# Kernel optimization log

Hardware: AMD Instinct MI355X
Metric: run time of the kernel (lower is better)

Reference implementation:

```python
import jax, jax.numpy as jnp
import numpy as np

N = 50000      # node_size
D = 256        # node_F == rel_F (ent_F)
R = 1000       # rel_size
E = 300000     # triple_size == n_edges
DEPTH = 2
KSEL = E // 2  # rows rewritten by W_orth transform
NPROXY = 128


def l2n(x):
    # tf.nn.l2_normalize with eps=1e-12
    return x * jax.lax.rsqrt(jnp.maximum(jnp.sum(x * x, axis=-1, keepdims=True), 1e-12))


def setup_inputs() -> dict:
    key = jax.random.key(0)
    ks = jax.random.split(key, 12)
    features = jax.random.normal(ks[0], (N, D), jnp.float32)
    rel_emb = jax.random.normal(ks[1], (R, D), jnp.float32)
    p = jax.random.normal(ks[2], (N, 1), jnp.float32)            # dynamic_node_kernel
    w_keys = jax.random.normal(ks[3], (DEPTH, D, D), jnp.float32) / np.float32(np.sqrt(D))
    attn_kernels = jax.random.normal(ks[4], (DEPTH, D, 1), jnp.float32) * 0.1
    proxy = jax.random.normal(ks[5], (NPROXY, D * (DEPTH + 1)), jnp.float32) * 0.05
    gate_kernel = jax.random.normal(ks[6], (D * (DEPTH + 1), D * (DEPTH + 1)), jnp.float32) / np.float32(np.sqrt(D * (DEPTH + 1)))
    adj_row = jnp.sort(jax.random.randint(ks[7], (E,), 0, N))    # destination (segment) ids, sorted
    adj_col = jax.random.randint(ks[8], (E,), 0, N)              # neighbor ids
    rel_ids = jax.random.randint(ks[9], (E,), 0, R)              # relation id per triple/edge
    rel_vals = jax.random.uniform(ks[10], (E,), jnp.float32)     # sparse_val per triple
    new_indices = jax.random.randint(ks[11], (KSEL,), 0, E)      # rows updated by w_key
    return dict(features=features, rel_emb=rel_emb, p=p, w_keys=w_keys,
                attn_kernels=attn_kernels, proxy=proxy, gate_kernel=gate_kernel,
                rel_vals=rel_vals, adj_row=adj_row, adj_col=adj_col,
                rel_ids=rel_ids, new_indices=new_indices)


def reference(features, rel_emb, p, w_keys, attn_kernels, proxy, gate_kernel,
              rel_vals, adj_row, adj_col, rel_ids, new_indices):
    tanh_p = jnp.tanh(p)                                   # [N,1]
    feats = features * tanh_p                              # use_p scaling (activation=None -> identity)
    outputs = [feats]
    for l in range(DEPTH):
        # sparse (triple,rel) x rel_emb : one relation per triple -> gather + scale
        rels_sum = rel_vals[:, None] * rel_emb[rel_ids]    # [E,D]
        rels_sum = l2n(rels_sum)
        # W_orth: transform a subset of rows by w_key, scatter back
        src = rels_sum[new_indices] @ w_keys[l]            # [KSEL,D]
        rels_sum = rels_sum.at[new_indices].set(src)
        neighs = feats[adj_col]                            # [E,D] gather
        rels_sum = rels_sum * tanh_p[adj_col]              # use_p on neighbors
        # Householder-style reflection of neighbor features
        neighs = neighs - 2.0 * jnp.sum(neighs * rels_sum, axis=1, keepdims=True) * rels_sum
        # per-edge attention logits, softmax over incoming edges of each row node
        att = (rels_sum @ attn_kernels[l])[:, 0]           # [E]
        m = jax.ops.segment_max(att, adj_row, num_segments=N)      # [N]
        att = jnp.exp(att - m[adj_row])
        s = jax.ops.segment_sum(att, adj_row, num_segments=N)      # [N]
        att = att / s[adj_row]
        # weighted scatter-aggregate
        feats = jax.ops.segment_sum(neighs * att[:, None], adj_row, num_segments=N)  # [N,D]
        feats = feats * tanh_p
        outputs.append(feats)
    out = jnp.concatenate(outputs, axis=-1)                # [N, D*(DEPTH+1)]
    proxy_att = jax.nn.softmax(l2n(out) @ l2n(proxy).T, axis=-1)   # [N,128]
    proxy_feature = out - proxy_att @ proxy
    gate = jax.nn.sigmoid(proxy_feature @ gate_kernel)
    out = gate * out + (1.0 - gate) * proxy_feature
    return (out, p)
```

## Files before the change

### kernel.cpp

```cpp
#include <hip/hip_runtime.h>
#include <math.h>

#define D 256
#define DCAT 768
#define NPX 128
#define QSTR 896
#define CSTR 136

typedef __attribute__((ext_vector_type(8))) short bf16x8;
typedef __attribute__((ext_vector_type(4))) float f32x4;

__device__ __forceinline__ short cvt_bf16(float f){
  union { float f; unsigned u; } v; v.f = f;
  unsigned r = v.u + 0x7FFF + ((v.u >> 16) & 1);
  return (short)(r >> 16);
}
__device__ __forceinline__ float bf2f(short s){
  union { float f; unsigned u; } v; v.u = ((unsigned)(unsigned short)s) << 16;
  return v.f;
}

__device__ __forceinline__ float waveSum(float v){
#pragma unroll
  for(int o=32;o>=1;o>>=1) v += __shfl_xor(v,o,64);
  return v;
}
__device__ __forceinline__ float waveMax(float v){
#pragma unroll
  for(int o=32;o>=1;o>>=1) v = fmaxf(v,__shfl_xor(v,o,64));
  return v;
}

__global__ void k_prep(const float* __restrict__ p, float* __restrict__ tp,
                       const int* __restrict__ adj_row, int* __restrict__ rs,
                       const int* __restrict__ idx, unsigned char* __restrict__ flag,
                       int n, int e, int ksel){
  int i = blockIdx.x*blockDim.x+threadIdx.x;
  if(i<n) tp[i]=tanhf(p[i]);
  if(i<=n){
    int lo=0, hi=e;
    while(lo<hi){ int mid=(lo+hi)>>1; if(adj_row[mid]<i) lo=mid+1; else hi=mid; }
    rs[i]=lo;
  }
  if(i<ksel) flag[idx[i]] = 1;
}

__global__ void k_relprep(const float* __restrict__ rel_emb, const float* __restrict__ attn,
                          float* __restrict__ ss_rel, float* __restrict__ att_n,
                          short* __restrict__ reb, int R_){
  __shared__ float sm[4];
  int r = blockIdx.x; int d = threadIdx.x;
  float v = rel_emb[(size_t)r*D+d];
  reb[(size_t)r*D+d] = cvt_bf16(v);
  int lane=threadIdx.x&63, wid=threadIdx.x>>6;
  float s = waveSum(v*v);
  if(lane==0) sm[wid]=s;
  __syncthreads();
  if(threadIdx.x==0) ss_rel[r]=sm[0]+sm[1]+sm[2]+sm[3];
  __syncthreads();
  for(int l=0;l<2;l++){
    float dd = waveSum(v*attn[l*D+d]);
    if(lane==0) sm[wid]=dd;
    __syncthreads();
    if(threadIdx.x==0) att_n[(size_t)l*R_+r]=sm[0]+sm[1]+sm[2]+sm[3];
    __syncthreads();
  }
}

__global__ void k_relW(const float* __restrict__ rel_emb, const float* __restrict__ W,
                       const float* __restrict__ ak, short* __restrict__ rwb,
                       float* __restrict__ att_t, int R_){
  __shared__ float sm[4];
  int r=blockIdx.x, d=threadIdx.x;
  const float* row = rel_emb + (size_t)r*D;
  float acc=0.f;
#pragma unroll 4
  for(int k=0;k<D;k++) acc = fmaf(row[k], W[(size_t)k*D+d], acc);
  rwb[(size_t)r*D+d]=cvt_bf16(acc);
  int lane=threadIdx.x&63, wid=threadIdx.x>>6;
  float dd = waveSum(acc*ak[d]);
  if(lane==0) sm[wid]=dd;
  __syncthreads();
  if(threadIdx.x==0) att_t[r]=sm[0]+sm[1]+sm[2]+sm[3];
}

__global__ void k_init0(const float* __restrict__ features, const float* __restrict__ tp,
                        short* __restrict__ Q, long total){
  long i = (long)blockIdx.x*blockDim.x+threadIdx.x;
  if(i >= total) return;
  int row = (int)(i>>8), d = (int)(i&255);
  Q[(size_t)row*QSTR + d] = cvt_bf16(features[i]*tp[row]);
}

__global__ void k_agg(const int* __restrict__ rs, const int* __restrict__ adj_col,
                      const int* __restrict__ rel_ids, const float* __restrict__ rel_vals,
                      const unsigned char* __restrict__ flag, const float* __restrict__ tp,
                      const float* __restrict__ ss_rel, const float* __restrict__ att_n,
                      const float* __restrict__ att_t, const short* __restrict__ reb,
                      const short* __restrict__ rwb, short* __restrict__ Q,
                      int n, int layer){
  int wid = threadIdx.x>>6, lane = threadIdx.x&63;
  int node = blockIdx.x*4 + wid;
  if(node>=n) return;
  int s = rs[node], e = rs[node+1];
  float accq[16];
#pragma unroll
  for(int k=0;k<16;k++) accq[k]=0.f;
  if(e > s){
    float mx = -INFINITY;
    for(int i=s+lane;i<e;i+=64){
      int rid = rel_ids[i]; float rv = rel_vals[i];
      float a = 0.f;
      if(rv>0.f){
        float t = tp[adj_col[i]];
        float sc = rv*rsqrtf(fmaxf(rv*rv*ss_rel[rid],1e-12f));
        a = t*sc*(flag[i]? att_t[rid] : att_n[rid]);
      }
      mx = fmaxf(mx,a);
    }
    mx = waveMax(mx);
    float se = 0.f;
    for(int i=s+lane;i<e;i+=64){
      int rid = rel_ids[i]; float rv = rel_vals[i];
      float a = 0.f;
      if(rv>0.f){
        float t = tp[adj_col[i]];
        float sc = rv*rsqrtf(fmaxf(rv*rv*ss_rel[rid],1e-12f));
        a = t*sc*(flag[i]? att_t[rid] : att_n[rid]);
      }
      se += __expf(a-mx);
    }
    se = waveSum(se);
    float inv = 1.f/se;
    int qid = lane>>4, ql = lane&15;
    for(int i0=s; i0<e; i0+=4){
      int j = i0 + qid;
      float w=0.f, coef=0.f;
      float nbv[16], rbv[16];
#pragma unroll
      for(int k=0;k<16;k++){ nbv[k]=0.f; rbv[k]=0.f; }
      if(j < e){
        int rid = rel_ids[j]; float rv = rel_vals[j]; int col = adj_col[j];
        const short* np = Q + (size_t)col*QSTR + layer*D + ql*16;
        bf16x8 n0 = *(const bf16x8*)np;
        bf16x8 n1 = *(const bf16x8*)(np+8);
#pragma unroll
        for(int k=0;k<8;k++){ nbv[k]=bf2f(n0[k]); nbv[k+8]=bf2f(n1[k]); }
        if(rv>0.f){
          float t = tp[col];
          float sc = rv*rsqrtf(fmaxf(rv*rv*ss_rel[rid],1e-12f));
          bool f = flag[j];
          const short* rp = (f? rwb : reb) + (size_t)rid*D + ql*16;
          bf16x8 r0 = *(const bf16x8*)rp;
          bf16x8 r1 = *(const bf16x8*)(rp+8);
#pragma unroll
          for(int k=0;k<8;k++){ rbv[k]=bf2f(r0[k]); rbv[k+8]=bf2f(r1[k]); }
          float dp = 0.f;
#pragma unroll
          for(int k=0;k<16;k++) dp += nbv[k]*rbv[k];
#pragma unroll
          for(int o=1;o<16;o<<=1) dp += __shfl_xor(dp,o,64);
          float a = t*sc*(f? att_t[rid] : att_n[rid]);
          w = __expf(a-mx)*inv;
          coef = 2.f*t*t*sc*sc*dp;
        } else {
          w = __expf(-mx)*inv;
        }
      }
#pragma unroll
      for(int k=0;k<16;k++) accq[k] += w*(nbv[k] - coef*rbv[k]);
    }
  }
#pragma unroll
  for(int k=0;k<16;k++){
    float v = accq[k];
    v += __shfl_xor(v,16,64);
    v += __shfl_xor(v,32,64);
    accq[k] = v;
  }
  if((lane>>4)==0){
    float t0 = tp[node];
    bf16x8 o0, o1;
#pragma unroll
    for(int k=0;k<8;k++){ o0[k]=cvt_bf16(accq[k]*t0); o1[k]=cvt_bf16(accq[k+8]*t0); }
    short* op = Q + (size_t)node*QSTR + (layer+1)*D + (lane&15)*16;
    *(bf16x8*)op = o0;
    *(bf16x8*)(op+8) = o1;
  }
}

__global__ void k_proxynorm(const float* __restrict__ proxy, short* __restrict__ pn){
  __shared__ float sm[4];
  int j = blockIdx.x;
  float ssum=0.f;
  for(int d=threadIdx.x; d<DCAT; d+=256){ float v=proxy[(size_t)j*DCAT+d]; ssum+=v*v; }
  int lane=threadIdx.x&63, wid=threadIdx.x>>6;
  ssum = waveSum(ssum);
  if(lane==0) sm[wid]=ssum;
  __syncthreads();
  float scale = rsqrtf(fmaxf(sm[0]+sm[1]+sm[2]+sm[3],1e-12f));
  for(int d=threadIdx.x; d<DCAT; d+=256)
    pn[(size_t)j*DCAT + d] = cvt_bf16(proxy[(size_t)j*DCAT+d]*scale);
}

__global__ void k_cast(const float* __restrict__ in, short* __restrict__ out, long total){
  long i = (long)blockIdx.x*blockDim.x+threadIdx.x;
  if(i<total) out[i]=cvt_bf16(in[i]);
}

__global__ void k_tcast(const float* __restrict__ in, short* __restrict__ out,
                        int R, int C, int ldo, int coff, float sign){
  __shared__ float tile[32][33];
  int bx = blockIdx.x*32, by = blockIdx.y*32;
  for(int i=threadIdx.y;i<32;i+=8){
    int rr = by+i, cc = bx+threadIdx.x;
    if(rr<R && cc<C) tile[i][threadIdx.x] = in[(size_t)rr*C + cc];
  }
  __syncthreads();
  for(int i=threadIdx.y;i<32;i+=8){
    int cc = bx+i, rr = by+threadIdx.x;
    if(cc<C && rr<R) out[(size_t)cc*ldo + coff + rr] = cvt_bf16(sign*tile[threadIdx.x][i]);
  }
}

__global__ void k_sn(const short* __restrict__ Q, float* __restrict__ sn, int n){
  int wid=threadIdx.x>>6, lane=threadIdx.x&63;
  int row = blockIdx.x*4+wid; if(row>=n) return;
  const short* o = Q + (size_t)row*QSTR;
  float ss=0.f;
#pragma unroll
  for(int c=0;c<3;c++){
    short4 v = *(const short4*)(o + c*256 + lane*4);
    float a=bf2f(v.x),b=bf2f(v.y),cc=bf2f(v.z),d=bf2f(v.w);
    ss += a*a+b*b+cc*cc+d*d;
  }
  ss = waveSum(ss);
  if(lane==0) sn[row]=rsqrtf(fmaxf(ss,1e-12f));
}

template<int LDA_, int LDB_, int NTOT, int KC>
__global__ __launch_bounds__(256,2) void k_gemm(
    const short* __restrict__ A, const short* __restrict__ Bt,
    float* __restrict__ outF, int M)
{
  __shared__ short smem[3][2][128*32];
  const int tid = threadIdx.x;
  const int lane = tid & 63, w = tid >> 6;
  const int wm = w >> 1, wn = w & 1;
  const int bn = blockIdx.x * 128, bm = blockIdx.y * 128;

  const short* Ag = A  + (size_t)bm * LDA_;
  const short* Bg = Bt + (size_t)bn * LDB_;

  auto stage = [&](int buf, int k0){
#pragma unroll
    for(int c=0;c<2;++c){
      int u = c*256 + tid;
      int row = u >> 2;
      int cb = ((u & 3) ^ ((u >> 3) & 3)) * 8;
      __builtin_amdgcn_global_load_lds(
        (const __attribute__((address_space(1))) unsigned int*)(Ag + (size_t)row*LDA_ + k0 + cb),
        (__attribute__((address_space(3))) unsigned int*)&smem[buf][0][u*8], 16, 0, 0);
      __builtin_amdgcn_global_load_lds(
        (const __attribute__((address_space(1))) unsigned int*)(Bg + (size_t)row*LDB_ + k0 + cb),
        (__attribute__((address_space(3))) unsigned int*)&smem[buf][1][u*8], 16, 0, 0);
    }
  };

  f32x4 acc[4][4] = {};
  const int lr = lane & 15, kg = lane >> 4;
  const int ksw = (kg ^ ((lr >> 1) & 3)) * 8;
  constexpr int NT = KC / 32;

  stage(0, 0);
  stage(1, 32);
  for(int t=0; t<NT; ++t){
    if(t+1 < NT) asm volatile("s_waitcnt vmcnt(4)" ::: "memory");
    else         asm volatile("s_waitcnt vmcnt(0)" ::: "memory");
    __builtin_amdgcn_s_barrier();
    __builtin_amdgcn_sched_barrier(0);
    const short* Al = &smem[t%3][0][0];
    const short* Bl = &smem[t%3][1][0];
    bf16x8 af[4], bfr[4];
#pragma unroll
    for(int i=0;i<4;++i) af[i] = *(const bf16x8*)(Al + (wm*64 + i*16 + lr)*32 + ksw);
#pragma unroll
    for(int j=0;j<4;++j) bfr[j] = *(const bf16x8*)(Bl + (wn*64 + j*16 + lr)*32 + ksw);
    if(t+2 < NT) stage((t+2)%3, (t+2)*32);
    __builtin_amdgcn_s_setprio(1);
#pragma unroll
    for(int i=0;i<4;++i)
#pragma unroll
      for(int j=0;j<4;++j)
        acc[i][j] = __builtin_amdgcn_mfma_f32_16x16x32_bf16(af[i], bfr[j], acc[i][j], 0, 0, 0);
    __builtin_amdgcn_s_setprio(0);
  }

  const int row0 = bm + wm*64 + (lane>>4)*4;
  const int col0 = bn + wn*64 + lr;
#pragma unroll
  for(int i=0;i<4;++i)
#pragma unroll
    for(int j=0;j<4;++j)
#pragma unroll
      for(int r=0;r<4;++r){
        int row = row0 + i*16 + r;
        if(row < M) outF[(size_t)row*NTOT + col0 + j*16] = acc[i][j][r];
      }
}

__global__ __launch_bounds__(256,2) void k_pr(
    short* __restrict__ Q, const short* __restrict__ pn,
    const float* __restrict__ sn, int M)
{
  __shared__ short smem[3][2][128*32];
  const int tid = threadIdx.x, lane = tid & 63, w = tid >> 6;
  const int wm = w >> 1, wn = w & 1;
  int nwg = gridDim.y;
  int orig = blockIdx.y;
  int q = nwg>>3, rm = nwg&7, xcd = orig&7, lid = orig>>3;
  int wg = (xcd<rm ? xcd*(q+1) : rm*(q+1)+(xcd-rm)*q) + lid;
  const int bm = wg*128;

  const short* Ag = Q + (size_t)bm * QSTR;
  const short* Bg = pn;

  auto stage = [&](int buf, int k0){
#pragma unroll
    for(int c=0;c<2;++c){
      int u = c*256 + tid;
      int row = u >> 2;
      int cb = ((u & 3) ^ ((u >> 3) & 3)) * 8;
      __builtin_amdgcn_global_load_lds(
        (const __attribute__((address_space(1))) unsigned int*)(Ag + (size_t)row*QSTR + k0 + cb),
        (__attribute__((address_space(3))) unsigned int*)&smem[buf][0][u*8], 16, 0, 0);
      __builtin_amdgcn_global_load_lds(
        (const __attribute__((address_space(1))) unsigned int*)(Bg + (size_t)row*DCAT + k0 + cb),
        (__attribute__((address_space(3))) unsigned int*)&smem[buf][1][u*8], 16, 0, 0);
    }
  };

  f32x4 acc[4][4] = {};
  const int lr = lane & 15, kg = lane >> 4;
  const int ksw = (kg ^ ((lr >> 1) & 3)) * 8;
  constexpr int NT = DCAT / 32;

  stage(0, 0);
  stage(1, 32);
  for(int t=0; t<NT; ++t){
    if(t+1 < NT) asm volatile("s_waitcnt vmcnt(4)" ::: "memory");
    else         asm volatile("s_waitcnt vmcnt(0)" ::: "memory");
    __builtin_amdgcn_s_barrier();
    __builtin_amdgcn_sched_barrier(0);
    const short* Al = &smem[t%3][0][0];
    const short* Bl = &smem[t%3][1][0];
    bf16x8 af[4], bfr[4];
#pragma unroll
    for(int i=0;i<4;++i) af[i] = *(const bf16x8*)(Al + (wm*64 + i*16 + lr)*32 + ksw);
#pragma unroll
    for(int j=0;j<4;++j) bfr[j] = *(const bf16x8*)(Bl + (wn*64 + j*16 + lr)*32 + ksw);
    if(t+2 < NT) stage((t+2)%3, (t+2)*32);
    __builtin_amdgcn_s_setprio(1);
#pragma unroll
    for(int i=0;i<4;++i)
#pragma unroll
      for(int j=0;j<4;++j)
        acc[i][j] = __builtin_amdgcn_mfma_f32_16x16x32_bf16(af[i], bfr[j], acc[i][j], 0, 0, 0);
    __builtin_amdgcn_s_setprio(0);
  }

  __syncthreads();
  short* lg = (short*)smem;
  const int row0l = wm*64 + kg*4;
  const int col0l = wn*64 + lr;
#pragma unroll
  for(int i=0;i<4;++i){
#pragma unroll
    for(int j=0;j<4;++j){
#pragma unroll
      for(int r=0;r<4;++r){
        int rl = row0l + i*16 + r;
        float s = sn[bm + rl];
        lg[rl*132 + col0l + j*16] = cvt_bf16(acc[i][j][r] * s);
      }
    }
  }
  __syncthreads();
  for(int k2=0;k2<32;++k2){
    int rl = w*32 + k2;
    float a = bf2f(lg[rl*132 + lane]);
    float b = bf2f(lg[rl*132 + 64 + lane]);
    float m = waveMax(fmaxf(a,b));
    float ea = __expf(a-m), eb = __expf(b-m);
    float sm_ = waveSum(ea+eb);
    float inv = 1.f/sm_;
    size_t rg = (size_t)(bm + rl);
    Q[rg*QSTR + DCAT + lane]      = cvt_bf16(ea*inv);
    Q[rg*QSTR + DCAT + 64 + lane] = cvt_bf16(eb*inv);
  }
}

__global__ __launch_bounds__(256,2) void k_go(
    short* __restrict__ Q, const short* __restrict__ BG,
    const short* __restrict__ Bt2, float* __restrict__ outF, int M)
{
  __shared__ short smem[3][2][128*32];
  const int tid = threadIdx.x, lane = tid & 63, w = tid >> 6;
  const int wm = w >> 1, wn = w & 1;
  const int gx = gridDim.x;
  int nwg = gx*gridDim.y;
  int orig = blockIdx.y*gx + blockIdx.x;
  int q = nwg>>3, rm = nwg&7, xcd = orig&7, lid = orig>>3;
  int wg = (xcd<rm ? xcd*(q+1) : rm*(q+1)+(xcd-rm)*q) + lid;
  const int bn = (wg%gx)*128, bm = (wg/gx)*128;
  const int lr = lane & 15, kg = lane >> 4;

  const short* Ag = Q  + (size_t)bm * QSTR;
  const short* Bg = BG + (size_t)bn * QSTR;

  auto stage = [&](int buf, int k0){
#pragma unroll
    for(int c=0;c<2;++c){
      int u = c*256 + tid;
      int row = u >> 2;
      int cb = ((u & 3) ^ ((u >> 3) & 3)) * 8;
      __builtin_amdgcn_global_load_lds(
        (const __attribute__((address_space(1))) unsigned int*)(Ag + (size_t)row*QSTR + k0 + cb),
        (__attribute__((address_space(3))) unsigned int*)&smem[buf][0][u*8], 16, 0, 0);
      __builtin_amdgcn_global_load_lds(
        (const __attribute__((address_space(1))) unsigned int*)(Bg + (size_t)row*QSTR + k0 + cb),
        (__attribute__((address_space(3))) unsigned int*)&smem[buf][1][u*8], 16, 0, 0);
    }
  };

  stage(0, 0);
  stage(1, 32);

  f32x4 acc[4][4] = {};
#pragma unroll
  for(int ks=0; ks<4; ++ks){
    bf16x8 af[4], bb[4];
#pragma unroll
    for(int i=0;i<4;++i)
      af[i] = *(const bf16x8*)(Q + (size_t)(bm + wm*64 + i*16 + lr)*QSTR + DCAT + ks*32 + kg*8);
#pragma unroll
    for(int j=0;j<4;++j)
      bb[j] = *(const bf16x8*)(Bt2 + (size_t)(bn + wn*64 + j*16 + lr)*NPX + ks*32 + kg*8);
#pragma unroll
    for(int i=0;i<4;++i)
#pragma unroll
      for(int j=0;j<4;++j)
        acc[i][j] = __builtin_amdgcn_mfma_f32_16x16x32_bf16(af[i], bb[j], acc[i][j], 0, 0, 0);
  }
  short4 pvb[4][4];
#pragma unroll
  for(int i=0;i<4;++i)
#pragma unroll
    for(int j=0;j<4;++j){
      pvb[i][j].x = cvt_bf16(acc[i][j][0]);
      pvb[i][j].y = cvt_bf16(acc[i][j][1]);
      pvb[i][j].z = cvt_bf16(acc[i][j][2]);
      pvb[i][j].w = cvt_bf16(acc[i][j][3]);
      acc[i][j] = (f32x4){0.f,0.f,0.f,0.f};
    }

  const int ksw = (kg ^ ((lr >> 1) & 3)) * 8;
  constexpr int NT = QSTR / 32;
  for(int t=0; t<NT; ++t){
    if(t+1 < NT) asm volatile("s_waitcnt vmcnt(4)" ::: "memory");
    else         asm volatile("s_waitcnt vmcnt(0)" ::: "memory");
    __builtin_amdgcn_s_barrier();
    __builtin_amdgcn_sched_barrier(0);
    const short* Al = &smem[t%3][0][0];
    const short* Bl = &smem[t%3][1][0];
    bf16x8 af[4], bfr[4];
#pragma unroll
    for(int i=0;i<4;++i) af[i] = *(const bf16x8*)(Al + (wm*64 + i*16 + lr)*32 + ksw);
#pragma unroll
    for(int j=0;j<4;++j) bfr[j] = *(const bf16x8*)(Bl + (wn*64 + j*16 + lr)*32 + ksw);
    if(t+2 < NT) stage((t+2)%3, (t+2)*32);
    __builtin_amdgcn_s_setprio(1);
#pragma unroll
    for(int i=0;i<4;++i)
#pragma unroll
      for(int j=0;j<4;++j)
        acc[i][j] = __builtin_amdgcn_mfma_f32_16x16x32_bf16(af[i], bfr[j], acc[i][j], 0, 0, 0);
    __builtin_amdgcn_s_setprio(0);
  }

  __syncthreads();
  short* cst = (short*)smem;
  const int row0l = wm*64 + kg*4;
  const int col0l = wn*64 + lr;
#pragma unroll
  for(int i=0;i<4;++i){
#pragma unroll
    for(int j=0;j<4;++j){
      float pv4[4] = { bf2f(pvb[i][j].x), bf2f(pvb[i][j].y), bf2f(pvb[i][j].z), bf2f(pvb[i][j].w) };
#pragma unroll
      for(int r2=0;r2<4;++r2){
        float g = 1.f/(1.f+__expf(-acc[i][j][r2]));
        cst[(row0l + i*16 + r2)*CSTR + col0l + j*16] = cvt_bf16((1.f-g)*pv4[r2]);
      }
    }
  }
  __syncthreads();
  const int rl0 = tid>>4, c0 = (tid&15)*8;
#pragma unroll
  for(int rr=0; rr<8; ++rr){
    int rl = rl0 + rr*16;
    int rg = bm + rl;
    if(rg >= M) continue;
    bf16x8 c8  = *(const bf16x8*)(cst + rl*CSTR + c0);
    bf16x8 oc8 = *(const bf16x8*)(Q + (size_t)rg*QSTR + bn + c0);
    float ov[8];
#pragma unroll
    for(int k=0;k<8;k++) ov[k] = bf2f(oc8[k]) - bf2f(c8[k]);
    *(float4*)(outF + (size_t)rg*DCAT + bn + c0)     = make_float4(ov[0],ov[1],ov[2],ov[3]);
    *(float4*)(outF + (size_t)rg*DCAT + bn + c0 + 4) = make_float4(ov[4],ov[5],ov[6],ov[7]);
  }
}

__global__ void k_copyp(const float* __restrict__ p, float* __restrict__ out, int n){
  int i = blockIdx.x*blockDim.x+threadIdx.x;
  if(i<n) out[i]=p[i];
}

extern "C" void kernel_launch(void* const* d_in, const int* in_sizes, int n_in,
                              void* d_out, int out_size, void* d_ws, size_t ws_size,
                              hipStream_t stream){
  const float* features = (const float*)d_in[0];
  const float* rel_emb  = (const float*)d_in[1];
  const float* p        = (const float*)d_in[2];
  const float* w_keys   = (const float*)d_in[3];
  const float* attn     = (const float*)d_in[4];
  const float* proxy    = (const float*)d_in[5];
  const float* gatek    = (const float*)d_in[6];
  const float* rel_vals = (const float*)d_in[7];
  const int* adj_row    = (const int*)d_in[8];
  const int* adj_col    = (const int*)d_in[9];
  const int* rel_ids    = (const int*)d_in[10];
  const int* new_idx    = (const int*)d_in[11];

  const int n    = in_sizes[2];
  const int r    = in_sizes[1]/D;
  const int e    = in_sizes[7];
  const int ksel = in_sizes[11];
  const size_t Mpad = ((size_t)n + 127) & ~(size_t)127;

  char* ws = (char*)d_ws;
  size_t off=0;
  auto alloc=[&](size_t bytes)->void*{ void* pp = ws+off; off=(off+bytes+255)&~(size_t)255; return pp; };
  float* tp      = (float*)alloc((size_t)n*4);
  int*   rs      = (int*)alloc((size_t)(n+1)*4);
  unsigned char* flag = (unsigned char*)alloc((size_t)e);
  float* ss_rel  = (float*)alloc((size_t)r*4);
  float* att_n   = (float*)alloc((size_t)2*r*4);
  float* att_t   = (float*)alloc((size_t)2*r*4);
  short* reb     = (short*)alloc((size_t)r*D*2);
  short* rwb     = (short*)alloc((size_t)2*r*D*2);
  short* pn      = (short*)alloc((size_t)NPX*DCAT*2);
  short* proxyb  = (short*)alloc((size_t)NPX*DCAT*2);
  short* Bt2     = (short*)alloc((size_t)DCAT*NPX*2);
  short* BG      = (short*)alloc((size_t)DCAT*QSTR*2);
  float* MxF     = (float*)alloc((size_t)NPX*DCAT*4);
  float* sn      = (float*)alloc(Mpad*4);
  short* Q       = (short*)alloc(Mpad*QSTR*2);

  float* outF = (float*)d_out;
  float* pout = (float*)d_out + (size_t)n*DCAT;

  hipMemsetAsync(flag, 0, (size_t)e, stream);
  hipMemsetAsync(Q + (size_t)n*QSTR, 0, (Mpad-(size_t)n)*QSTR*2, stream);

  int prep_n = (ksel > n+1 ? ksel : n+1);
  k_prep<<<(prep_n+255)/256,256,0,stream>>>(p,tp,adj_row,rs,new_idx,flag,n,e,ksel);
  k_relprep<<<r,256,0,stream>>>(rel_emb,attn,ss_rel,att_n,reb,r);
  for(int l=0;l<2;l++)
    k_relW<<<r,256,0,stream>>>(rel_emb, w_keys+(size_t)l*D*D, attn+(size_t)l*D,
                               rwb+(size_t)l*r*D, att_t+(size_t)l*r, r);
  k_proxynorm<<<NPX,256,0,stream>>>(proxy,pn);
  {
    long tpx = (long)NPX*DCAT;
    k_cast<<<(int)((tpx+255)/256),256,0,stream>>>(proxy, proxyb, tpx);
    dim3 tb(32,8);
    k_tcast<<<dim3(DCAT/32, DCAT/32), tb, 0, stream>>>(gatek, BG, DCAT, DCAT, QSTR, 0, 1.f);
    k_gemm<DCAT, QSTR, DCAT, DCAT><<<dim3(DCAT/128,1),256,0,stream>>>(proxyb, BG, MxF, NPX);
    k_tcast<<<dim3(DCAT/32, NPX/32), tb, 0, stream>>>(MxF, BG, NPX, DCAT, QSTR, DCAT, -1.f);
    k_tcast<<<dim3(DCAT/32, NPX/32), tb, 0, stream>>>(proxy, Bt2, NPX, DCAT, NPX, 0, 1.f);
  }
  long tot0 = (long)n*D;
  k_init0<<<(int)((tot0+255)/256),256,0,stream>>>(features,tp,Q,tot0);
  for(int l=0;l<2;l++)
    k_agg<<<(n+3)/4,256,0,stream>>>(rs,adj_col,rel_ids,rel_vals,flag,tp,ss_rel,
                                    att_n+(size_t)l*r, att_t+(size_t)l*r, reb,
                                    rwb+(size_t)l*r*D, Q, n, l);
  k_sn<<<(n+3)/4,256,0,stream>>>(Q,sn,n);

  int mt = (int)(Mpad/128);
  k_pr<<<dim3(1, mt),256,0,stream>>>(Q, pn, sn, n);
  k_go<<<dim3(DCAT/128, mt),256,0,stream>>>(Q, BG, Bt2, outF, n);
  k_copyp<<<(n+255)/256,256,0,stream>>>(p,pout,n);
}
```

Baseline: 512.5 us.

## Enlarge gate GEMM tile to 256x256 with 512 threads, defer proxy matmul to epilogue

The final gate GEMM kernel now uses 256x256 output tiles with 8 waves per block instead of 128x128 with 4 waves. This raises operand reuse per LDS load and reduces how often the Q panel is re-read across column tiles. The proxy-attention product (att @ proxy) now runs in the epilogue, one half-tile at a time, instead of before the main loop, which keeps its accumulators out of the registers held during the loop. In exchange the block has a larger register footprint (32 accumulator tiles per wave) and more LDS, which may lower occupancy. Mpad is rounded to 256 and the scale read in k_pr is now bounds-checked for the extra padded rows.

```diff
diff --git a/kernel.cpp b/kernel.cpp
--- a/kernel.cpp
+++ b/kernel.cpp
@@ -5,7 +5,6 @@
 #define DCAT 768
 #define NPX 128
 #define QSTR 896
-#define CSTR 136
 
 typedef __attribute__((ext_vector_type(8))) short bf16x8;
 typedef __attribute__((ext_vector_type(4))) float f32x4;
@@ -380,7 +379,8 @@
 #pragma unroll
       for(int r=0;r<4;++r){
         int rl = row0l + i*16 + r;
-        float s = sn[bm + rl];
+        int rg = bm + rl;
+        float s = (rg < M) ? sn[rg] : 0.f;
         lg[rl*132 + col0l + j*16] = cvt_bf16(acc[i][j][r] * s);
       }
     }
@@ -400,20 +400,20 @@
   }
 }
 
-__global__ __launch_bounds__(256,2) void k_go(
-    short* __restrict__ Q, const short* __restrict__ BG,
+__global__ __launch_bounds__(512,2) void k_gate(
+    const short* __restrict__ Q, const short* __restrict__ BG,
     const short* __restrict__ Bt2, float* __restrict__ outF, int M)
 {
-  __shared__ short smem[3][2][128*32];
-  const int tid = threadIdx.x, lane = tid & 63, w = tid >> 6;
-  const int wm = w >> 1, wn = w & 1;
+  __shared__ short smem[3][2][256*32];
+  const int tid = threadIdx.x, lane = tid & 63, wid = tid >> 6;
+  const int wm = wid >> 2, wn = wid & 3;
+  const int lr = lane & 15, kg = lane >> 4;
   const int gx = gridDim.x;
   int nwg = gx*gridDim.y;
   int orig = blockIdx.y*gx + blockIdx.x;
   int q = nwg>>3, rm = nwg&7, xcd = orig&7, lid = orig>>3;
   int wg = (xcd<rm ? xcd*(q+1) : rm*(q+1)+(xcd-rm)*q) + lid;
-  const int bn = (wg%gx)*128, bm = (wg/gx)*128;
-  const int lr = lane & 15, kg = lane >> 4;
+  const int bn = (wg%gx)*256, bm = (wg/gx)*256;
 
   const short* Ag = Q  + (size_t)bm * QSTR;
   const short* Bg = BG + (size_t)bn * QSTR;
@@ -421,7 +421,7 @@
   auto stage = [&](int buf, int k0){
 #pragma unroll
     for(int c=0;c<2;++c){
-      int u = c*256 + tid;
+      int u = c*512 + tid;
       int row = u >> 2;
       int cb = ((u & 3) ^ ((u >> 3) & 3)) * 8;
       __builtin_amdgcn_global_load_lds(
@@ -433,39 +433,12 @@
     }
   };
 
+  f32x4 acc[8][4] = {};
+  const int ksw = (kg ^ ((lr >> 1) & 3)) * 8;
+  constexpr int NT = QSTR / 32;
+
   stage(0, 0);
   stage(1, 32);
-
-  f32x4 acc[4][4] = {};
-#pragma unroll
-  for(int ks=0; ks<4; ++ks){
-    bf16x8 af[4], bb[4];
-#pragma unroll
-    for(int i=0;i<4;++i)
-      af[i] = *(const bf16x8*)(Q + (size_t)(bm + wm*64 + i*16 + lr)*QSTR + DCAT + ks*32 + kg*8);
-#pragma unroll
-    for(int j=0;j<4;++j)
-      bb[j] = *(const bf16x8*)(Bt2 + (size_t)(bn + wn*64 + j*16 + lr)*NPX + ks*32 + kg*8);
-#pragma unroll
-    for(int i=0;i<4;++i)
-#pragma unroll
-      for(int j=0;j<4;++j)
-        acc[i][j] = __builtin_amdgcn_mfma_f32_16x16x32_bf16(af[i], bb[j], acc[i][j], 0, 0, 0);
-  }
-  short4 pvb[4][4];
-#pragma unroll
-  for(int i=0;i<4;++i)
-#pragma unroll
-    for(int j=0;j<4;++j){
-      pvb[i][j].x = cvt_bf16(acc[i][j][0]);
-      pvb[i][j].y = cvt_bf16(acc[i][j][1]);
-      pvb[i][j].z = cvt_bf16(acc[i][j][2]);
-      pvb[i][j].w = cvt_bf16(acc[i][j][3]);
-      acc[i][j] = (f32x4){0.f,0.f,0.f,0.f};
-    }
-
-  const int ksw = (kg ^ ((lr >> 1) & 3)) * 8;
-  constexpr int NT = QSTR / 32;
   for(int t=0; t<NT; ++t){
     if(t+1 < NT) asm volatile("s_waitcnt vmcnt(4)" ::: "memory");
     else         asm volatile("s_waitcnt vmcnt(0)" ::: "memory");
@@ -473,15 +446,16 @@
     __builtin_amdgcn_sched_barrier(0);
     const short* Al = &smem[t%3][0][0];
     const short* Bl = &smem[t%3][1][0];
-    bf16x8 af[4], bfr[4];
-#pragma unroll
-    for(int i=0;i<4;++i) af[i] = *(const bf16x8*)(Al + (wm*64 + i*16 + lr)*32 + ksw);
+    bf16x8 bfr[4];
 #pragma unroll
     for(int j=0;j<4;++j) bfr[j] = *(const bf16x8*)(Bl + (wn*64 + j*16 + lr)*32 + ksw);
+    bf16x8 af[8];
+#pragma unroll
+    for(int i=0;i<8;++i) af[i] = *(const bf16x8*)(Al + (wm*128 + i*16 + lr)*32 + ksw);
     if(t+2 < NT) stage((t+2)%3, (t+2)*32);
     __builtin_amdgcn_s_setprio(1);
 #pragma unroll
-    for(int i=0;i<4;++i)
+    for(int i=0;i<8;++i)
 #pragma unroll
       for(int j=0;j<4;++j)
         acc[i][j] = __builtin_amdgcn_mfma_f32_16x16x32_bf16(af[i], bfr[j], acc[i][j], 0, 0, 0);
@@ -490,34 +464,45 @@
 
   __syncthreads();
   short* cst = (short*)smem;
-  const int row0l = wm*64 + kg*4;
-  const int col0l = wn*64 + lr;
-#pragma unroll
-  for(int i=0;i<4;++i){
-#pragma unroll
-    for(int j=0;j<4;++j){
-      float pv4[4] = { bf2f(pvb[i][j].x), bf2f(pvb[i][j].y), bf2f(pvb[i][j].z), bf2f(pvb[i][j].w) };
-#pragma unroll
-      for(int r2=0;r2<4;++r2){
-        float g = 1.f/(1.f+__expf(-acc[i][j][r2]));
-        cst[(row0l + i*16 + r2)*CSTR + col0l + j*16] = cvt_bf16((1.f-g)*pv4[r2]);
-      }
-    }
-  }
-  __syncthreads();
-  const int rl0 = tid>>4, c0 = (tid&15)*8;
-#pragma unroll
-  for(int rr=0; rr<8; ++rr){
-    int rl = rl0 + rr*16;
-    int rg = bm + rl;
-    if(rg >= M) continue;
-    bf16x8 c8  = *(const bf16x8*)(cst + rl*CSTR + c0);
-    bf16x8 oc8 = *(const bf16x8*)(Q + (size_t)rg*QSTR + bn + c0);
-    float ov[8];
-#pragma unroll
-    for(int k=0;k<8;k++) ov[k] = bf2f(oc8[k]) - bf2f(c8[k]);
-    *(float4*)(outF + (size_t)rg*DCAT + bn + c0)     = make_float4(ov[0],ov[1],ov[2],ov[3]);
-    *(float4*)(outF + (size_t)rg*DCAT + bn + c0 + 4) = make_float4(ov[4],ov[5],ov[6],ov[7]);
+  for(int h=0; h<2; ++h){
+    if(wm == h){
+#pragma unroll
+      for(int i=0;i<8;++i){
+        f32x4 pv[4] = {};
+#pragma unroll
+        for(int ks=0;ks<4;++ks){
+          bf16x8 pa = *(const bf16x8*)(Q + (size_t)(bm + h*128 + i*16 + lr)*QSTR + DCAT + ks*32 + kg*8);
+#pragma unroll
+          for(int j=0;j<4;++j){
+            bf16x8 vb = *(const bf16x8*)(Bt2 + (size_t)(bn + wn*64 + j*16 + lr)*NPX + ks*32 + kg*8);
+            pv[j] = __builtin_amdgcn_mfma_f32_16x16x32_bf16(pa, vb, pv[j], 0, 0, 0);
+          }
+        }
+#pragma unroll
+        for(int j=0;j<4;++j)
+#pragma unroll
+          for(int r2=0;r2<4;++r2){
+            float g = 1.f/(1.f+__expf(-acc[i][j][r2]));
+            cst[(i*16 + kg*4 + r2)*264 + wn*64 + j*16 + lr] = cvt_bf16((1.f-g)*pv[j][r2]);
+          }
+      }
+    }
+    __syncthreads();
+    const int c0 = (tid & 31)*8;
+    for(int it=0; it<8; ++it){
+      int rl = (tid>>5) + it*16;
+      int rg = bm + h*128 + rl;
+      if(rg < M){
+        bf16x8 c8  = *(const bf16x8*)(cst + rl*264 + c0);
+        bf16x8 oc8 = *(const bf16x8*)(Q + (size_t)rg*QSTR + bn + c0);
+        float ov[8];
+#pragma unroll
+        for(int k=0;k<8;k++) ov[k] = bf2f(oc8[k]) - bf2f(c8[k]);
+        *(float4*)(outF + (size_t)rg*DCAT + bn + c0)     = make_float4(ov[0],ov[1],ov[2],ov[3]);
+        *(float4*)(outF + (size_t)rg*DCAT + bn + c0 + 4) = make_float4(ov[4],ov[5],ov[6],ov[7]);
+      }
+    }
+    __syncthreads();
   }
 }
 
@@ -546,7 +531,7 @@
   const int r    = in_sizes[1]/D;
   const int e    = in_sizes[7];
   const int ksel = in_sizes[11];
-  const size_t Mpad = ((size_t)n + 127) & ~(size_t)127;
+  const size_t Mpad = ((size_t)n + 255) & ~(size_t)255;
 
   char* ws = (char*)d_ws;
   size_t off=0;
@@ -599,6 +584,6 @@
 
   int mt = (int)(Mpad/128);
   k_pr<<<dim3(1, mt),256,0,stream>>>(Q, pn, sn, n);
-  k_go<<<dim3(DCAT/128, mt),256,0,stream>>>(Q, BG, Bt2, outF, n);
+  k_gate<<<dim3(DCAT/256, (int)(Mpad/256)),512,0,stream>>>(Q, BG, Bt2, outF, n);
   k_copyp<<<(n+255)/256,256,0,stream>>>(p,pout,n);
 }
```

Result: slower. 593.2 us (+15.8%).
